# Optimization experiments

Measured on AMD Instinct MI355X. Metric: run time of the kernel, lower is better.

Reference implementation:

```python
import jax, jax.numpy as jnp
import numpy as np

NUM_GRAPHS = 512


def setup_inputs() -> dict:
    key = jax.random.key(0)
    ks = jax.random.split(key, 16)
    N, E = 50000, 800000
    x = jax.random.normal(ks[0], (N, 3), dtype=jnp.float32)
    edge_index = jax.random.randint(ks[1], (2, E), 0, N, dtype=jnp.int64)
    batch = jnp.sort(jax.random.randint(ks[2], (N,), 0, NUM_GRAPHS, dtype=jnp.int64))

    def glorot(k, shape):
        fan_in, fan_out = shape
        lim = (6.0 / (fan_in + fan_out)) ** 0.5
        return jax.random.uniform(k, shape, jnp.float32, -lim, lim)

    return {
        "x": x, "edge_index": edge_index, "batch": batch,
        "W1": glorot(ks[3], (3, 32)),   "b1": jnp.zeros((32,), jnp.float32),
        "W2": glorot(ks[4], (32, 64)),  "b2": jnp.zeros((64,), jnp.float32),
        "W3": glorot(ks[5], (64, 128)), "b3": jnp.zeros((128,), jnp.float32),
        "Wf1": glorot(ks[6], (128, 32)), "bf1": jnp.zeros((32,), jnp.float32),
        "Wf2": glorot(ks[7], (32, 4)),   "bf2": jnp.zeros((4,), jnp.float32),
    }


def _gcn_conv(x, src, dst, norm, W, b, N):
    # GCNConv: h = x W, then symmetric-normalized aggregation, then bias.
    h = x @ W                                   # [N, out]
    msg = h[src] * norm[:, None]                # [E+N, out] gathered edge messages
    out = jax.ops.segment_sum(msg, dst, num_segments=N)
    return out + b


def reference(x, edge_index, batch, W1, b1, W2, b2, W3, b3, Wf1, bf1, Wf2, bf2):
    N = x.shape[0]
    loops = jnp.arange(N, dtype=edge_index.dtype)
    src = jnp.concatenate([edge_index[0], loops])   # add self-loops (GCNConv default)
    dst = jnp.concatenate([edge_index[1], loops])
    # symmetric normalization deg^-1/2[src] * deg^-1/2[dst], deg counted on dst
    deg = jax.ops.segment_sum(jnp.ones_like(dst, dtype=x.dtype), dst, num_segments=N)
    dinv = jnp.where(deg > 0, jax.lax.rsqrt(deg), 0.0)
    norm = dinv[src] * dinv[dst]                    # [E+N]

    h = jax.nn.relu(_gcn_conv(x, src, dst, norm, W1, b1, N))
    h = jax.nn.relu(_gcn_conv(h, src, dst, norm, W2, b2, N))
    h = jax.nn.relu(_gcn_conv(h, src, dst, norm, W3, b3, N))

    # global mean pool over graphs
    sums = jax.ops.segment_sum(h, batch, num_segments=NUM_GRAPHS)
    cnts = jax.ops.segment_sum(jnp.ones((N,), h.dtype), batch, num_segments=NUM_GRAPHS)
    pooled = sums / jnp.maximum(cnts, 1.0)[:, None]   # [G, 128]

    z = jax.nn.relu(pooled @ Wf1 + bf1)
    return z @ Wf2 + bf2                              # [G, 4]
```

## Files before the change

kernel.cpp:

```cpp
#include <hip/hip_runtime.h>

#define NN 50000
#define NE 800000
#define NG 512
#define CAP 64
#define NP 196
#define CH 3200
#define NCH 250

__global__ __launch_bounds__(256) void p1_hist_k(const int* __restrict__ dst,
                                                 int* __restrict__ Ht, int e) {
    __shared__ int lh[NP];
    int t = threadIdx.x, b = blockIdx.x;
    if (t < NP) lh[t] = 0;
    __syncthreads();
    int i0 = b * CH, i1 = min(e, i0 + CH);
    for (int i = i0 + t; i < i1; i += 256) atomicAdd(&lh[dst[i] >> 8], 1);
    __syncthreads();
    if (t < NP) Ht[t * NCH + b] = lh[t];
}

__global__ __launch_bounds__(256) void p2a_k(int* __restrict__ Ht, int* __restrict__ tot) {
    __shared__ int sh[256];
    int p = blockIdx.x, t = threadIdx.x;
    int v = (t < NCH) ? Ht[p * NCH + t] : 0;
    sh[t] = v;
    __syncthreads();
    for (int off = 1; off < 256; off <<= 1) {
        int x = (t >= off) ? sh[t - off] : 0;
        __syncthreads();
        sh[t] += x;
        __syncthreads();
    }
    if (t < NCH) Ht[p * NCH + t] = sh[t] - v;
    if (t == 255) tot[p] = sh[255];
}

__global__ __launch_bounds__(256) void p3_place_k(const int* __restrict__ src,
                                                  const int* __restrict__ dst,
                                                  const int* __restrict__ Ht,
                                                  const int* __restrict__ tot,
                                                  int* __restrict__ pak, int e) {
    __shared__ int cur[NP];
    __shared__ int sh[256];
    int t = threadIdx.x, b = blockIdx.x;
    int v = (t < NP) ? tot[t] : 0;
    sh[t] = v;
    __syncthreads();
    for (int off = 1; off < 256; off <<= 1) {
        int x = (t >= off) ? sh[t - off] : 0;
        __syncthreads();
        sh[t] += x;
        __syncthreads();
    }
    if (t < NP) cur[t] = (sh[t] - v) + Ht[t * NCH + b];
    __syncthreads();
    int i0 = b * CH, i1 = min(e, i0 + CH);
    for (int i = i0 + t; i < i1; i += 256) {
        int d = dst[i], s = src[i];
        int p = d >> 8, dl = d & 255;
        int pos = atomicAdd(&cur[p], 1);
        pak[pos] = s | (dl << 16);
    }
}

__global__ __launch_bounds__(256) void p4_build_k(const int* __restrict__ pak,
                                                  const int* __restrict__ tot,
                                                  const float* __restrict__ x,
                                                  int* __restrict__ fill,
                                                  float* __restrict__ dinv,
                                                  float* __restrict__ xs,
                                                  int* __restrict__ eidx, int n) {
    __shared__ int curn[256], sh[256];
    int p = blockIdx.x, t = threadIdx.x;
    curn[t] = 0;
    int v = (t < NP) ? tot[t] : 0;
    sh[t] = v;
    __syncthreads();
    for (int off = 1; off < 256; off <<= 1) {
        int x2 = (t >= off) ? sh[t - off] : 0;
        __syncthreads();
        sh[t] += x2;
        __syncthreads();
    }
    int s1 = sh[p];
    int s0 = s1 - tot[p];
    for (int i = s0 + t; i < s1; i += 256) {
        int w = pak[i];
        int dl = w >> 16, s = w & 0xFFFF;
        int pos = atomicAdd(&curn[dl], 1) & (CAP - 1);
        eidx[(size_t)(p * 256 + dl) * CAP + pos] = s;
    }
    __syncthreads();
    int node = p * 256 + t;
    if (node < n) {
        int dg = curn[t];
        fill[node] = dg;
        float d = rsqrtf((float)(dg + 1));
        dinv[node] = d;
        float4 vv;
        vv.x = x[node * 3 + 0] * d;
        vv.y = x[node * 3 + 1] * d;
        vv.z = x[node * 3 + 2] * d;
        vv.w = 0.0f;
        *(float4*)(xs + (size_t)node * 4) = vv;
    }
}

__device__ __forceinline__ unsigned short f2bf_rn(float f) {
    unsigned int u = __float_as_uint(f);
    u += 0x7FFFu + ((u >> 16) & 1u);
    return (unsigned short)(u >> 16);
}

__global__ __launch_bounds__(256) void fused_l1_k(
    const int* __restrict__ deg, const int* __restrict__ eidx,
    const float* __restrict__ xs, const float* __restrict__ W1,
    const float* __restrict__ b1, const float* __restrict__ dinv,
    float* __restrict__ A2, unsigned short* __restrict__ A2b, int n) {
    __shared__ float act[64][4];
    int t = threadIdx.x;
    int node0 = blockIdx.x * 64;
    {
        int node = node0 + (t >> 2);
        int f = t & 3;
        if (node < n) {
            int e1 = deg[node];
            const int* __restrict__ eb = eidx + node * CAP;
            float acc = xs[(size_t)node * 4 + f];
            int e = 0;
            for (; e + 4 <= e1; e += 4) {
                int4 s = *(const int4*)(eb + e);
                float v0 = xs[(size_t)s.x * 4 + f];
                float v1 = xs[(size_t)s.y * 4 + f];
                float v2 = xs[(size_t)s.z * 4 + f];
                float v3 = xs[(size_t)s.w * 4 + f];
                acc += (v0 + v1) + (v2 + v3);
            }
            for (; e < e1; ++e) acc += xs[(size_t)eb[e] * 4 + f];
            act[t >> 2][f] = acc;
        }
    }
    __syncthreads();
    int f = t & 31;
    int nl0 = t >> 5;
#pragma unroll
    for (int i = 0; i < 8; ++i) {
        int nl = nl0 + i * 8;
        int node = node0 + nl;
        if (node < n) {
            float acc = act[nl][0] * W1[f] + act[nl][1] * W1[32 + f] + act[nl][2] * W1[64 + f];
            float s = dinv[node];
            float o = fmaxf(fmaf(s, acc, b1[f]), 0.0f) * s;
            A2[(size_t)node * 32 + f] = o;
            A2b[(size_t)node * 32 + f] = f2bf_rn(o);
        }
    }
}

template <int F>
__global__ __launch_bounds__(256) void gatherbf_k(const int* __restrict__ deg,
                                                  const int* __restrict__ eidx,
                                                  const float* __restrict__ Aself,
                                                  const uint4* __restrict__ Ab,
                                                  float* __restrict__ B, int n) {
    constexpr int FV = F / 8;
    constexpr int NPB = 256 / FV;
    constexpr int RU4 = F / 8;
    int t = threadIdx.x;
    int node = blockIdx.x * NPB + t / FV;
    int j = (t % FV) * 8;
    if (node >= n) return;
    int e1 = deg[node];
    const int* __restrict__ eb = eidx + (size_t)node * CAP;
    const uint4* __restrict__ Aj = Ab + (j >> 3);
    float4 p0 = *(const float4*)(Aself + (size_t)node * F + j);
    float4 p1 = *(const float4*)(Aself + (size_t)node * F + j + 4);
    float4 q0 = make_float4(0.f, 0.f, 0.f, 0.f);
    float4 q1 = make_float4(0.f, 0.f, 0.f, 0.f);
#define BF_UNPACK8(u, lo, hi)                                                 \
    {                                                                         \
        lo.x += __uint_as_float((u).x << 16);                                 \
        lo.y += __uint_as_float((u).x & 0xFFFF0000u);                         \
        lo.z += __uint_as_float((u).y << 16);                                 \
        lo.w += __uint_as_float((u).y & 0xFFFF0000u);                         \
        hi.x += __uint_as_float((u).z << 16);                                 \
        hi.y += __uint_as_float((u).z & 0xFFFF0000u);                         \
        hi.z += __uint_as_float((u).w << 16);                                 \
        hi.w += __uint_as_float((u).w & 0xFFFF0000u);                         \
    }
    int e = 0;
    for (; e + 16 <= e1; e += 16) {
        int4 sa = *(const int4*)(eb + e);
        int4 sb = *(const int4*)(eb + e + 4);
        int4 sc = *(const int4*)(eb + e + 8);
        int4 sd = *(const int4*)(eb + e + 12);
        uint4 v0 = Aj[(size_t)sa.x * RU4];
        uint4 v1 = Aj[(size_t)sa.y * RU4];
        uint4 v2 = Aj[(size_t)sa.z * RU4];
        uint4 v3 = Aj[(size_t)sa.w * RU4];
        uint4 v4 = Aj[(size_t)sb.x * RU4];
        uint4 v5 = Aj[(size_t)sb.y * RU4];
        uint4 v6 = Aj[(size_t)sb.z * RU4];
        uint4 v7 = Aj[(size_t)sb.w * RU4];
        uint4 v8 = Aj[(size_t)sc.x * RU4];
        uint4 v9 = Aj[(size_t)sc.y * RU4];
        uint4 va = Aj[(size_t)sc.z * RU4];
        uint4 vb = Aj[(size_t)sc.w * RU4];
        uint4 vc = Aj[(size_t)sd.x * RU4];
        uint4 vd = Aj[(size_t)sd.y * RU4];
        uint4 ve = Aj[(size_t)sd.z * RU4];
        uint4 vf = Aj[(size_t)sd.w * RU4];
        BF_UNPACK8(v0, p0, p1) BF_UNPACK8(v1, q0, q1)
        BF_UNPACK8(v2, p0, p1) BF_UNPACK8(v3, q0, q1)
        BF_UNPACK8(v4, p0, p1) BF_UNPACK8(v5, q0, q1)
        BF_UNPACK8(v6, p0, p1) BF_UNPACK8(v7, q0, q1)
        BF_UNPACK8(v8, p0, p1) BF_UNPACK8(v9, q0, q1)
        BF_UNPACK8(va, p0, p1) BF_UNPACK8(vb, q0, q1)
        BF_UNPACK8(vc, p0, p1) BF_UNPACK8(vd, q0, q1)
        BF_UNPACK8(ve, p0, p1) BF_UNPACK8(vf, q0, q1)
    }
    for (; e + 4 <= e1; e += 4) {
        int4 sa = *(const int4*)(eb + e);
        uint4 v0 = Aj[(size_t)sa.x * RU4];
        uint4 v1 = Aj[(size_t)sa.y * RU4];
        uint4 v2 = Aj[(size_t)sa.z * RU4];
        uint4 v3 = Aj[(size_t)sa.w * RU4];
        BF_UNPACK8(v0, p0, p1) BF_UNPACK8(v1, q0, q1)
        BF_UNPACK8(v2, p0, p1) BF_UNPACK8(v3, q0, q1)
    }
    for (; e < e1; ++e) {
        uint4 v = Aj[(size_t)eb[e] * RU4];
        BF_UNPACK8(v, p0, p1)
    }
#undef BF_UNPACK8
    p0.x += q0.x; p0.y += q0.y; p0.z += q0.z; p0.w += q0.w;
    p1.x += q1.x; p1.y += q1.y; p1.z += q1.z; p1.w += q1.w;
    *(float4*)(B + (size_t)node * F + j) = p0;
    *(float4*)(B + (size_t)node * F + j + 4) = p1;
}

template <int Fin, int Fout, int NPB, bool SCALE_OUT, bool WRITE_F32, bool WRITE_BF>
__global__ __launch_bounds__(256) void mmB_k(
    const float* __restrict__ G, const float* __restrict__ W,
    const float* __restrict__ bias, const float* __restrict__ dinv,
    float* __restrict__ Aout, unsigned short* __restrict__ Abf, int n) {
    constexpr int FL = Fout / 4;
    constexpr int NGRP = 256 / FL;
    constexpr int NPT = NPB / NGRP;
    __shared__ float act[NPB][Fin];
    int t = threadIdx.x;
    int node0 = blockIdx.x * NPB;
    constexpr int TOT4 = NPB * Fin / 4;
    const float4* __restrict__ G4 = (const float4*)(G + (size_t)node0 * Fin);
    float4* act4 = (float4*)&act[0][0];
    for (int i = t; i < TOT4; i += 256) {
        int nl = i / (Fin / 4);
        float4 v = make_float4(0.f, 0.f, 0.f, 0.f);
        if (node0 + nl < n) v = G4[i];
        act4[i] = v;
    }
    __syncthreads();
    int f4 = (t % FL) * 4;
    int nlbase = (t / FL) * NPT;
    float4 acc[NPT];
#pragma unroll
    for (int i = 0; i < NPT; ++i) acc[i] = make_float4(0.f, 0.f, 0.f, 0.f);
    for (int k = 0; k < Fin; k += 4) {
        float4 a[NPT];
#pragma unroll
        for (int i = 0; i < NPT; ++i) a[i] = *(const float4*)&act[nlbase + i][k];
#pragma unroll
        for (int kk = 0; kk < 4; ++kk) {
            float4 w = *(const float4*)(W + (size_t)(k + kk) * Fout + f4);
#pragma unroll
            for (int i = 0; i < NPT; ++i) {
                float av = (&a[i].x)[kk];
                acc[i].x = fmaf(av, w.x, acc[i].x);
                acc[i].y = fmaf(av, w.y, acc[i].y);
                acc[i].z = fmaf(av, w.z, acc[i].z);
                acc[i].w = fmaf(av, w.w, acc[i].w);
            }
        }
    }
    float4 bv = *(const float4*)(bias + f4);
#pragma unroll
    for (int i = 0; i < NPT; ++i) {
        int node = node0 + nlbase + i;
        if (node < n) {
            float s = dinv[node];
            float4 o;
            o.x = fmaxf(fmaf(s, acc[i].x, bv.x), 0.0f);
            o.y = fmaxf(fmaf(s, acc[i].y, bv.y), 0.0f);
            o.z = fmaxf(fmaf(s, acc[i].z, bv.z), 0.0f);
            o.w = fmaxf(fmaf(s, acc[i].w, bv.w), 0.0f);
            if (SCALE_OUT) { o.x *= s; o.y *= s; o.z *= s; o.w *= s; }
            if (WRITE_F32) *(float4*)(Aout + (size_t)node * Fout + f4) = o;
            if (WRITE_BF) {
                ushort4 ob;
                ob.x = f2bf_rn(o.x); ob.y = f2bf_rn(o.y);
                ob.z = f2bf_rn(o.z); ob.w = f2bf_rn(o.w);
                *(ushort4*)(Abf + (size_t)node * Fout + f4) = ob;
            }
        }
    }
}

__device__ __forceinline__ int lbound_d(const int* __restrict__ a, int n, int key) {
    int lo = 0, hi = n;
    while (lo < hi) {
        int m = (lo + hi) >> 1;
        if (a[m] < key) lo = m + 1; else hi = m;
    }
    return lo;
}

__global__ __launch_bounds__(128) void poolhead_k(
    const unsigned short* __restrict__ Hb, const int* __restrict__ batch,
    const float* __restrict__ Wf1, const float* __restrict__ bf1,
    const float* __restrict__ Wf2, const float* __restrict__ bf2,
    float* __restrict__ out, int n) {
    __shared__ int bnd[2];
    __shared__ float pm[128];
    __shared__ float z[32];
    int g = blockIdx.x, t = threadIdx.x;
    if (t == 0) bnd[0] = lbound_d(batch, n, g);
    if (t == 1) bnd[1] = lbound_d(batch, n, g + 1);
    __syncthreads();
    int lo = bnd[0], hi = bnd[1];
    float s0 = 0.f, s1 = 0.f, s2 = 0.f, s3 = 0.f;
    int i = lo;
    for (; i + 4 <= hi; i += 4) {
        s0 += __uint_as_float((unsigned)Hb[(size_t)i * 128 + t] << 16);
        s1 += __uint_as_float((unsigned)Hb[(size_t)(i + 1) * 128 + t] << 16);
        s2 += __uint_as_float((unsigned)Hb[(size_t)(i + 2) * 128 + t] << 16);
        s3 += __uint_as_float((unsigned)Hb[(size_t)(i + 3) * 128 + t] << 16);
    }
    for (; i < hi; ++i) s0 += __uint_as_float((unsigned)Hb[(size_t)i * 128 + t] << 16);
    float c = (float)(hi - lo);
    c = fmaxf(c, 1.0f);
    pm[t] = ((s0 + s1) + (s2 + s3)) / c;
    __syncthreads();
    if (t < 32) {
        float acc = bf1[t];
#pragma unroll 4
        for (int k = 0; k < 128; ++k) acc = fmaf(pm[k], Wf1[k * 32 + t], acc);
        z[t] = fmaxf(acc, 0.0f);
    }
    __syncthreads();
    if (t < 4) {
        float acc = bf2[t];
#pragma unroll
        for (int jj = 0; jj < 32; ++jj) acc = fmaf(z[jj], Wf2[jj * 4 + t], acc);
        out[g * 4 + t] = acc;
    }
}

extern "C" void kernel_launch(void* const* d_in, const int* in_sizes, int n_in,
                              void* d_out, int out_size, void* d_ws, size_t ws_size,
                              hipStream_t stream) {
    const float* x    = (const float*)d_in[0];
    const int*   ei   = (const int*)d_in[1];
    const int*   batch= (const int*)d_in[2];
    const float* W1   = (const float*)d_in[3];
    const float* b1   = (const float*)d_in[4];
    const float* W2   = (const float*)d_in[5];
    const float* b2   = (const float*)d_in[6];
    const float* W3   = (const float*)d_in[7];
    const float* b3   = (const float*)d_in[8];
    const float* Wf1  = (const float*)d_in[9];
    const float* bf1  = (const float*)d_in[10];
    const float* Wf2  = (const float*)d_in[11];
    const float* bf2  = (const float*)d_in[12];
    float* out = (float*)d_out;

    int*   fill   = (int*)d_ws;
    float* dinv   = (float*)(fill + NN);
    float* xs     = dinv + NN;
    float* A2     = xs + (size_t)NN * 4;
    float* A3     = A2 + (size_t)NN * 32;
    float* G      = A3 + (size_t)NN * 64;
    int*   eidx   = (int*)(G + (size_t)NN * 64);
    unsigned short* A2b = (unsigned short*)(eidx + (size_t)NN * CAP);
    unsigned short* A3b = A2b + (size_t)NN * 32;
    unsigned short* H3b = A3b + (size_t)NN * 64;

    int* pak = (int*)G;
    int* Ht  = (int*)H3b;
    int* tot = Ht + NP * NCH;

    const int* src = ei;
    const int* dst = ei + NE;

    p1_hist_k<<<NCH, 256, 0, stream>>>(dst, Ht, NE);
    p2a_k<<<NP, 256, 0, stream>>>(Ht, tot);
    p3_place_k<<<NCH, 256, 0, stream>>>(src, dst, Ht, tot, pak, NE);
    p4_build_k<<<NP, 256, 0, stream>>>(pak, tot, x, fill, dinv, xs, eidx, NN);

    fused_l1_k<<<(NN + 63) / 64, 256, 0, stream>>>(
        fill, eidx, xs, W1, b1, dinv, A2, A2b, NN);

    gatherbf_k<32><<<(NN + 63) / 64, 256, 0, stream>>>(
        fill, eidx, A2, (const uint4*)A2b, G, NN);
    mmB_k<32, 64, 32, true, true, true><<<(NN + 31) / 32, 256, 0, stream>>>(
        G, W2, b2, dinv, A3, A3b, NN);

    gatherbf_k<64><<<(NN + 31) / 32, 256, 0, stream>>>(
        fill, eidx, A3, (const uint4*)A3b, G, NN);
    mmB_k<64, 128, 32, false, false, true><<<(NN + 31) / 32, 256, 0, stream>>>(
        G, W3, b3, dinv, nullptr, H3b, NN);

    poolhead_k<<<NG, 128, 0, stream>>>(H3b, batch, Wf1, bf1, Wf2, bf2, out, NN);
}
```

Measured before the change: 205.2 us.

## Replace two-level counting-sort graph build with direct global-atomic bucket fill

Drops the four-kernel partitioned counting sort (histogram, scan, place, per-partition build) used to build the per-node neighbour lists. Instead it zeroes the fill counters and has each edge atomically claim a slot in its destination's fixed-capacity row, then a separate node pass computes dinv and scaled features and clamps the count. This cuts kernel launches and the intermediate packed buffer, at the cost of contended global atomics and scattered writes into the bucket rows. It also changes overflow semantics: the old code wrapped slot indices modulo the capacity, while the new code drops edges past the capacity but still counts them in the degree.

After: 229.1 us. +11.6%, slower.

```diff
diff --git a/kernel.cpp b/kernel.cpp
--- a/kernel.cpp
+++ b/kernel.cpp
@@ -4,107 +4,34 @@
 #define NE 800000
 #define NG 512
 #define CAP 64
-#define NP 196
-#define CH 3200
-#define NCH 250
-
-__global__ __launch_bounds__(256) void p1_hist_k(const int* __restrict__ dst,
-                                                 int* __restrict__ Ht, int e) {
-    __shared__ int lh[NP];
-    int t = threadIdx.x, b = blockIdx.x;
-    if (t < NP) lh[t] = 0;
-    __syncthreads();
-    int i0 = b * CH, i1 = min(e, i0 + CH);
-    for (int i = i0 + t; i < i1; i += 256) atomicAdd(&lh[dst[i] >> 8], 1);
-    __syncthreads();
-    if (t < NP) Ht[t * NCH + b] = lh[t];
-}
-
-__global__ __launch_bounds__(256) void p2a_k(int* __restrict__ Ht, int* __restrict__ tot) {
-    __shared__ int sh[256];
-    int p = blockIdx.x, t = threadIdx.x;
-    int v = (t < NCH) ? Ht[p * NCH + t] : 0;
-    sh[t] = v;
-    __syncthreads();
-    for (int off = 1; off < 256; off <<= 1) {
-        int x = (t >= off) ? sh[t - off] : 0;
-        __syncthreads();
-        sh[t] += x;
-        __syncthreads();
-    }
-    if (t < NCH) Ht[p * NCH + t] = sh[t] - v;
-    if (t == 255) tot[p] = sh[255];
-}
-
-__global__ __launch_bounds__(256) void p3_place_k(const int* __restrict__ src,
-                                                  const int* __restrict__ dst,
-                                                  const int* __restrict__ Ht,
-                                                  const int* __restrict__ tot,
-                                                  int* __restrict__ pak, int e) {
-    __shared__ int cur[NP];
-    __shared__ int sh[256];
-    int t = threadIdx.x, b = blockIdx.x;
-    int v = (t < NP) ? tot[t] : 0;
-    sh[t] = v;
-    __syncthreads();
-    for (int off = 1; off < 256; off <<= 1) {
-        int x = (t >= off) ? sh[t - off] : 0;
-        __syncthreads();
-        sh[t] += x;
-        __syncthreads();
-    }
-    if (t < NP) cur[t] = (sh[t] - v) + Ht[t * NCH + b];
-    __syncthreads();
-    int i0 = b * CH, i1 = min(e, i0 + CH);
-    for (int i = i0 + t; i < i1; i += 256) {
-        int d = dst[i], s = src[i];
-        int p = d >> 8, dl = d & 255;
-        int pos = atomicAdd(&cur[p], 1);
-        pak[pos] = s | (dl << 16);
-    }
-}
-
-__global__ __launch_bounds__(256) void p4_build_k(const int* __restrict__ pak,
-                                                  const int* __restrict__ tot,
-                                                  const float* __restrict__ x,
-                                                  int* __restrict__ fill,
-                                                  float* __restrict__ dinv,
-                                                  float* __restrict__ xs,
-                                                  int* __restrict__ eidx, int n) {
-    __shared__ int curn[256], sh[256];
-    int p = blockIdx.x, t = threadIdx.x;
-    curn[t] = 0;
-    int v = (t < NP) ? tot[t] : 0;
-    sh[t] = v;
-    __syncthreads();
-    for (int off = 1; off < 256; off <<= 1) {
-        int x2 = (t >= off) ? sh[t - off] : 0;
-        __syncthreads();
-        sh[t] += x2;
-        __syncthreads();
-    }
-    int s1 = sh[p];
-    int s0 = s1 - tot[p];
-    for (int i = s0 + t; i < s1; i += 256) {
-        int w = pak[i];
-        int dl = w >> 16, s = w & 0xFFFF;
-        int pos = atomicAdd(&curn[dl], 1) & (CAP - 1);
-        eidx[(size_t)(p * 256 + dl) * CAP + pos] = s;
-    }
-    __syncthreads();
-    int node = p * 256 + t;
-    if (node < n) {
-        int dg = curn[t];
-        fill[node] = dg;
-        float d = rsqrtf((float)(dg + 1));
-        dinv[node] = d;
-        float4 vv;
-        vv.x = x[node * 3 + 0] * d;
-        vv.y = x[node * 3 + 1] * d;
-        vv.z = x[node * 3 + 2] * d;
-        vv.w = 0.0f;
-        *(float4*)(xs + (size_t)node * 4) = vv;
-    }
+
+__global__ __launch_bounds__(256) void build_k(const int* __restrict__ src,
+                                               const int* __restrict__ dst,
+                                               int* __restrict__ fill,
+                                               int* __restrict__ eidx, int e) {
+    int i = blockIdx.x * 256 + threadIdx.x;
+    if (i >= e) return;
+    int d = dst[i], s = src[i];
+    int pos = atomicAdd(&fill[d], 1);
+    if (pos < CAP) eidx[(size_t)d * CAP + pos] = s;
+}
+
+__global__ __launch_bounds__(256) void node_init_k(int* __restrict__ fill,
+                                                   const float* __restrict__ x,
+                                                   float* __restrict__ dinv,
+                                                   float* __restrict__ xs, int n) {
+    int node = blockIdx.x * 256 + threadIdx.x;
+    if (node >= n) return;
+    int dg = fill[node];
+    float d = rsqrtf((float)(dg + 1));
+    dinv[node] = d;
+    if (dg > CAP) fill[node] = CAP;
+    float4 v;
+    v.x = x[node * 3 + 0] * d;
+    v.y = x[node * 3 + 1] * d;
+    v.z = x[node * 3 + 2] * d;
+    v.w = 0.0f;
+    *(float4*)(xs + (size_t)node * 4) = v;
 }
 
 __device__ __forceinline__ unsigned short f2bf_rn(float f) {
@@ -385,17 +312,12 @@
     unsigned short* A3b = A2b + (size_t)NN * 32;
     unsigned short* H3b = A3b + (size_t)NN * 64;
 
-    int* pak = (int*)G;
-    int* Ht  = (int*)H3b;
-    int* tot = Ht + NP * NCH;
-
     const int* src = ei;
     const int* dst = ei + NE;
 
-    p1_hist_k<<<NCH, 256, 0, stream>>>(dst, Ht, NE);
-    p2a_k<<<NP, 256, 0, stream>>>(Ht, tot);
-    p3_place_k<<<NCH, 256, 0, stream>>>(src, dst, Ht, tot, pak, NE);
-    p4_build_k<<<NP, 256, 0, stream>>>(pak, tot, x, fill, dinv, xs, eidx, NN);
+    hipMemsetAsync(fill, 0, NN * sizeof(int), stream);
+    build_k<<<(NE + 255) / 256, 256, 0, stream>>>(src, dst, fill, eidx, NE);
+    node_init_k<<<(NN + 255) / 256, 256, 0, stream>>>(fill, x, dinv, xs, NN);
 
     fused_l1_k<<<(NN + 63) / 64, 256, 0, stream>>>(
         fill, eidx, xs, W1, b1, dinv, A2, A2b, NN);
```
